# Optimization experiments

Hardware: AMD Instinct MI355X
Metric: run time of the kernel (lower is better)

Reference implementation:

```python
import jax, jax.numpy as jnp
import numpy as np

BLOCK = 128          # per-block quantization group size (BLOCK_SIZE in source)
FP8_MAX = 448.0      # max representable magnitude of float8_e4m3fn


def _quantize(x2d):
    # Per-128-element block quantization along the last (contiguous) dim,
    # matching quantize_fp8_triton applied to the row-major flattened tensor.
    R, K = x2d.shape
    xb = x2d.reshape(R, K // BLOCK, BLOCK)
    s = jnp.max(jnp.abs(xb), axis=-1) / FP8_MAX            # [R, K//BLOCK] fp32 scales
    y = (xb / s[..., None]).astype(jnp.float8_e4m3fn)      # fp8 payload
    return y, s


def _dequantize(y, s):
    # Inline dequant: fp8 -> fp32 times per-block scale (fused into GEMM accum in the kernel).
    return (y.astype(jnp.float32) * s[..., None]).reshape(y.shape[0], -1)


def setup_inputs() -> dict:
    key = jax.random.key(0)
    kx, kw = jax.random.split(key)
    B, T, D, O = 4, 2048, 4096, 4096
    x = jax.random.normal(kx, (B, T, D), dtype=jnp.float32)
    limit = float(np.sqrt(6.0 / (D + O)))  # xavier_uniform_
    weight = jax.random.uniform(kw, (O, D), minval=-limit, maxval=limit, dtype=jnp.float32)
    return {"x": x, "weight": weight}


def reference(x, weight):
    B, T, D = x.shape
    xf = x.reshape(-1, D)                  # [M, K]
    xq, xs = _quantize(xf)                 # fp8 activations + per-(row,kblock) scales
    wq, ws = _quantize(weight)             # fp8 weights + per-(row,kblock) scales
    # Block-scaled GEMM: sum_i (A_i @ B_i^T) * a_s[:, i] * b_s[:, i]
    # expressed equivalently as dequant-then-matmul (identical math, fp32 accumulate).
    out = _dequantize(xq, xs) @ _dequantize(wq, ws).T      # [M, N]
    return out.reshape(B, T, -1)
```

## Files before the change

kernel.cpp:

```cpp
#include <hip/hip_runtime.h>

using u16 = unsigned short;
typedef int i32x4 __attribute__((ext_vector_type(4)));
typedef int i32x8 __attribute__((ext_vector_type(8)));
typedef float f32x4 __attribute__((ext_vector_type(4)));
typedef float f32x2 __attribute__((ext_vector_type(2)));
typedef float f32x16 __attribute__((ext_vector_type(16)));

#define SC1 0x7F7F7F7F

__device__ inline void async16(const void* g, void* l) {
    __builtin_amdgcn_global_load_lds(
        (__attribute__((address_space(1))) void*)(g),
        (__attribute__((address_space(3))) void*)(l),
        16, 0, 0);
}

__device__ inline i32x8 mk8(i32x4 lo, i32x4 hi) {
    return __builtin_shufflevector(lo, hi, 0, 1, 2, 3, 4, 5, 6, 7);
}

__global__ void quant_kernel(const float* __restrict__ in,
                             u16* __restrict__ outq,
                             float* __restrict__ outs,
                             long R) {
    long wid = (long)blockIdx.x * 4 + (threadIdx.x >> 6);
    int lane = threadIdx.x & 63;
    if (wid >= R * 32) return;

    float2 v = reinterpret_cast<const float2*>(in + wid * 128)[lane];
    float a = fmaxf(fabsf(v.x), fabsf(v.y));
#pragma unroll
    for (int off = 32; off; off >>= 1) a = fmaxf(a, __shfl_xor(a, off));

    float s = a / 448.0f;
    float qx = v.x / s;
    float qy = v.y / s;
    qx = fminf(fmaxf(qx, -448.0f), 448.0f);
    qy = fminf(fmaxf(qy, -448.0f), 448.0f);

    int pk = __builtin_amdgcn_cvt_pk_fp8_f32(qx, qy, 0, false);
    outq[wid * 64 + lane] = (u16)(pk & 0xFFFF);

    if (lane == 0) {
        long row = wid >> 5, kb = wid & 31;
        outs[kb * R + row] = s;
    }
}


#define SWZ(x) ((x) ^ ((((x) >> 7) & 7) << 4))

#define FENCE asm volatile("" ::: "memory");
#define BARRIER { __builtin_amdgcn_s_barrier(); FENCE }
#define VMC0 { asm volatile("s_waitcnt vmcnt(0)" ::: "memory"); }

__global__ __launch_bounds__(256, 2) void gemm_fp8(
    const char* __restrict__ Aq, const char* __restrict__ Bq,
    const float* __restrict__ AscaleG, const float* __restrict__ BscaleG,
    float* __restrict__ C, int M, int N) {
    extern __shared__ __align__(16) char smem[];
    const int KBYTES = 4096;

    const int tid = threadIdx.x;
    const int wid = tid >> 6;
    const int lane = tid & 63;
    const int l31 = lane & 31;
    const int lh = lane >> 5;
    const int wr2 = wid >> 1;
    const int wc2 = wid & 1;

    int nwg = gridDim.x, bid = blockIdx.x, swz = bid;
    if ((nwg & 7) == 0) swz = (bid & 7) * (nwg >> 3) + (bid >> 3);
    const int nbn = N >> 7;
    const long brow = (long)(swz / nbn) << 7;
    const long bcol = (long)(swz % nbn) << 7;

    const char* Abase = Aq + brow * KBYTES;
    const char* Bbase = Bq + bcol * KBYTES;

    int aofs[4];
#pragma unroll
    for (int c = 0; c < 4; ++c) {
        int dloc = c * 4096 + tid * 16;
        int l = SWZ(dloc);
        aofs[c] = (l >> 7) * KBYTES + (l & 127);
    }

    int cox[4];
#pragma unroll
    for (int kh = 0; kh < 2; ++kh)
#pragma unroll
        for (int hh = 0; hh < 2; ++hh)
            cox[kh * 2 + hh] =
                (((kh << 6) | (lh << 5) | (hh << 4)) ^ ((lane & 7) << 4));

    int arowb[2], brownn[2];
#pragma unroll
    for (int rb = 0; rb < 2; ++rb) arowb[rb] = (wr2 * 64 + rb * 32 + l31) << 7;
#pragma unroll
    for (int n = 0; n < 2; ++n) brownn[n] = (wc2 * 64 + n * 32 + l31) << 7;

#define STAGE(kb1) { int bufb_ = (kb1) & 1; \
    _Pragma("unroll") for (int c_ = 0; c_ < 4; ++c_) { \
        char* dA_ = smem + bufb_ * 16384 + c_ * 4096 + wid * 1024; \
        async16(Abase + aofs[c_] + (long)(kb1) * 128, dA_); \
        async16(Bbase + aofs[c_] + (long)(kb1) * 128, dA_ + 32768); } \
    if (wid == 0 && lane < 32) \
        async16((const char*)AscaleG + ((long)(kb1) * M + brow) * 4 + lane * 16, \
                smem + 65536 + bufb_ * 512); \
    if (wid == 1 && lane < 32) \
        async16((const char*)BscaleG + ((long)(kb1) * N + bcol) * 4 + lane * 16, \
                smem + 66560 + bufb_ * 512); }

    f32x16 acc[2][2];
#pragma unroll
    for (int rb = 0; rb < 2; ++rb)
#pragma unroll
        for (int n = 0; n < 2; ++n)
#pragma unroll
            for (int e = 0; e < 16; ++e) acc[rb][n][e] = 0.f;

    STAGE(0);
    VMC0; BARRIER;

    for (int kb = 0; kb < 32; ++kb) {
        const int buf = kb & 1;
        if (kb < 31) STAGE(kb + 1);

        const char* Ab = smem + buf * 16384;
        const char* Bb = smem + 32768 + buf * 16384;
        const float* Sa = (const float*)(smem + 65536 + buf * 512);
        const float* Sb = (const float*)(smem + 66560 + buf * 512);

        i32x8 bfr[2][2];
#pragma unroll
        for (int n = 0; n < 2; ++n)
#pragma unroll
            for (int kh = 0; kh < 2; ++kh)
                bfr[n][kh] = mk8(*(const i32x4*)(Bb + brownn[n] + cox[kh * 2]),
                                 *(const i32x4*)(Bb + brownn[n] + cox[kh * 2 + 1]));
        float sbv[2];
#pragma unroll
        for (int n = 0; n < 2; ++n) sbv[n] = Sb[wc2 * 64 + n * 32 + l31];

#pragma unroll
        for (int rb = 0; rb < 2; ++rb) {
            i32x8 a0 = mk8(*(const i32x4*)(Ab + arowb[rb] + cox[0]),
                           *(const i32x4*)(Ab + arowb[rb] + cox[1]));
            i32x8 a1 = mk8(*(const i32x4*)(Ab + arowb[rb] + cox[2]),
                           *(const i32x4*)(Ab + arowb[rb] + cox[3]));
            f32x4 sa4[4];
#pragma unroll
            for (int i = 0; i < 4; ++i)
                sa4[i] = *(const f32x4*)(Sa + wr2 * 64 + rb * 32 + 4 * lh + 8 * i);
            __builtin_amdgcn_s_setprio(1);
            f32x16 t0 = __builtin_amdgcn_mfma_scale_f32_32x32x64_f8f6f4(
                a0, bfr[0][0], (f32x16)(0.f), 0, 0, 0, SC1, 0, SC1);
            t0 = __builtin_amdgcn_mfma_scale_f32_32x32x64_f8f6f4(
                a1, bfr[0][1], t0, 0, 0, 0, SC1, 0, SC1);
            f32x16 t1 = __builtin_amdgcn_mfma_scale_f32_32x32x64_f8f6f4(
                a0, bfr[1][0], (f32x16)(0.f), 0, 0, 0, SC1, 0, SC1);
            t1 = __builtin_amdgcn_mfma_scale_f32_32x32x64_f8f6f4(
                a1, bfr[1][1], t1, 0, 0, 0, SC1, 0, SC1);
            __builtin_amdgcn_s_setprio(0);
#pragma unroll
            for (int i = 0; i < 4; ++i)
#pragma unroll
                for (int j = 0; j < 4; ++j) {
                    acc[rb][0][i * 4 + j] = fmaf(t0[i * 4 + j],
                        sa4[i][j] * sbv[0], acc[rb][0][i * 4 + j]);
                    acc[rb][1][i * 4 + j] = fmaf(t1[i * 4 + j],
                        sa4[i][j] * sbv[1], acc[rb][1][i * 4 + j]);
                }
        }

        VMC0; BARRIER;
    }

#pragma unroll
    for (int rb = 0; rb < 2; ++rb)
#pragma unroll
        for (int n = 0; n < 2; ++n)
#pragma unroll
            for (int e = 0; e < 16; ++e) {
                long r = brow + wr2 * 64 + rb * 32 + (e & 3) + 8 * (e >> 2) + 4 * lh;
                long cc = bcol + wc2 * 64 + n * 32 + l31;
                C[r * (long)N + cc] = acc[rb][n][e];
            }
#undef STAGE
}

extern "C" void kernel_launch(void* const* d_in, const int* in_sizes, int n_in,
                              void* d_out, int out_size, void* d_ws, size_t ws_size,
                              hipStream_t stream) {
    const float* x = (const float*)d_in[0];
    const float* w = (const float*)d_in[1];
    float* out = (float*)d_out;

    const int K = 4096;
    const long M = (long)in_sizes[0] / K;
    const long N = (long)in_sizes[1] / K;

    u16* Aq = (u16*)d_ws;
    u16* Bq = Aq + (size_t)M * K / 2;
    float* Asc = (float*)(Bq + (size_t)N * K / 2);
    float* Bsc = Asc + 32 * (size_t)M;

    const long nblkA = M * 32, nblkB = N * 32;
    quant_kernel<<<dim3((unsigned)((nblkA + 3) / 4)), dim3(256), 0, stream>>>(
        x, Aq, Asc, M);
    quant_kernel<<<dim3((unsigned)((nblkB + 3) / 4)), dim3(256), 0, stream>>>(
        w, Bq, Bsc, N);

    static int smem_set = 0;
    if (!smem_set) {
        hipFuncSetAttribute((const void*)gemm_fp8,
                            hipFuncAttributeMaxDynamicSharedMemorySize, 67584);
        smem_set = 1;
    }
    dim3 grid((unsigned)((M / 128) * (N / 128)));
    gemm_fp8<<<grid, dim3(256), 67584, stream>>>(
        (const char*)Aq, (const char*)Bq, Asc, Bsc, out, (int)M, (int)N);
}
```

Before: 275.0 us.

## Shrink GEMM tile to 128x64, fuse quant launches, raise occupancy

After: 300.8 us. +9.4%, slower.

```diff
diff --git a/kernel.cpp b/kernel.cpp
--- a/kernel.cpp
+++ b/kernel.cpp
@@ -20,15 +20,20 @@
     return __builtin_shufflevector(lo, hi, 0, 1, 2, 3, 4, 5, 6, 7);
 }
 
-__global__ void quant_kernel(const float* __restrict__ in,
-                             u16* __restrict__ outq,
-                             float* __restrict__ outs,
-                             long R) {
+__global__ void quant_kernel(const float* __restrict__ x,
+                             const float* __restrict__ w,
+                             u16* __restrict__ Aq, u16* __restrict__ Bq,
+                             float* __restrict__ Asc, float* __restrict__ Bsc,
+                             long nA, long nTot, long MM, long NN) {
     long wid = (long)blockIdx.x * 4 + (threadIdx.x >> 6);
     int lane = threadIdx.x & 63;
-    if (wid >= R * 32) return;
-
-    float2 v = reinterpret_cast<const float2*>(in + wid * 128)[lane];
+    if (wid >= nTot) return;
+
+    const float* in; u16* outq; float* outs; long R, id;
+    if (wid < nA) { in = x; outq = Aq; outs = Asc; R = MM; id = wid; }
+    else          { in = w; outq = Bq; outs = Bsc; R = NN; id = wid - nA; }
+
+    float2 v = reinterpret_cast<const float2*>(in + id * 128)[lane];
     float a = fmaxf(fabsf(v.x), fabsf(v.y));
 #pragma unroll
     for (int off = 32; off; off >>= 1) a = fmaxf(a, __shfl_xor(a, off));
@@ -40,10 +45,10 @@
     qy = fminf(fmaxf(qy, -448.0f), 448.0f);
 
     int pk = __builtin_amdgcn_cvt_pk_fp8_f32(qx, qy, 0, false);
-    outq[wid * 64 + lane] = (u16)(pk & 0xFFFF);
+    outq[id * 64 + lane] = (u16)(pk & 0xFFFF);
 
     if (lane == 0) {
-        long row = wid >> 5, kb = wid & 31;
+        long row = id >> 5, kb = id & 31;
         outs[kb * R + row] = s;
     }
 }
@@ -55,7 +60,7 @@
 #define BARRIER { __builtin_amdgcn_s_barrier(); FENCE }
 #define VMC0 { asm volatile("s_waitcnt vmcnt(0)" ::: "memory"); }
 
-__global__ __launch_bounds__(256, 2) void gemm_fp8(
+__global__ __launch_bounds__(256, 3) void gemm_fp8(
     const char* __restrict__ Aq, const char* __restrict__ Bq,
     const float* __restrict__ AscaleG, const float* __restrict__ BscaleG,
     float* __restrict__ C, int M, int N) {
@@ -72,9 +77,9 @@
 
     int nwg = gridDim.x, bid = blockIdx.x, swz = bid;
     if ((nwg & 7) == 0) swz = (bid & 7) * (nwg >> 3) + (bid >> 3);
-    const int nbn = N >> 7;
+    const int nbn = N >> 6;
     const long brow = (long)(swz / nbn) << 7;
-    const long bcol = (long)(swz % nbn) << 7;
+    const long bcol = (long)(swz % nbn) << 6;
 
     const char* Abase = Aq + brow * KBYTES;
     const char* Bbase = Bq + bcol * KBYTES;
@@ -95,31 +100,30 @@
             cox[kh * 2 + hh] =
                 (((kh << 6) | (lh << 5) | (hh << 4)) ^ ((lane & 7) << 4));
 
-    int arowb[2], brownn[2];
+    int arowb[2];
 #pragma unroll
     for (int rb = 0; rb < 2; ++rb) arowb[rb] = (wr2 * 64 + rb * 32 + l31) << 7;
-#pragma unroll
-    for (int n = 0; n < 2; ++n) brownn[n] = (wc2 * 64 + n * 32 + l31) << 7;
+    const int brown = (wc2 * 32 + l31) << 7;
 
 #define STAGE(kb1) { int bufb_ = (kb1) & 1; \
     _Pragma("unroll") for (int c_ = 0; c_ < 4; ++c_) { \
         char* dA_ = smem + bufb_ * 16384 + c_ * 4096 + wid * 1024; \
-        async16(Abase + aofs[c_] + (long)(kb1) * 128, dA_); \
-        async16(Bbase + aofs[c_] + (long)(kb1) * 128, dA_ + 32768); } \
+        async16(Abase + aofs[c_] + (long)(kb1) * 128, dA_); } \
+    _Pragma("unroll") for (int c_ = 0; c_ < 2; ++c_) { \
+        char* dB_ = smem + 32768 + bufb_ * 8192 + c_ * 4096 + wid * 1024; \
+        async16(Bbase + aofs[c_] + (long)(kb1) * 128, dB_); } \
     if (wid == 0 && lane < 32) \
         async16((const char*)AscaleG + ((long)(kb1) * M + brow) * 4 + lane * 16, \
-                smem + 65536 + bufb_ * 512); \
-    if (wid == 1 && lane < 32) \
+                smem + 49152 + bufb_ * 512); \
+    if (wid == 3 && lane < 16) \
         async16((const char*)BscaleG + ((long)(kb1) * N + bcol) * 4 + lane * 16, \
-                smem + 66560 + bufb_ * 512); }
-
-    f32x16 acc[2][2];
+                smem + 50176 + bufb_ * 256); }
+
+    f32x2 acc2[2][8];
 #pragma unroll
     for (int rb = 0; rb < 2; ++rb)
 #pragma unroll
-        for (int n = 0; n < 2; ++n)
-#pragma unroll
-            for (int e = 0; e < 16; ++e) acc[rb][n][e] = 0.f;
+        for (int p = 0; p < 8; ++p) acc2[rb][p] = (f32x2){0.f, 0.f};
 
     STAGE(0);
     VMC0; BARRIER;
@@ -129,20 +133,16 @@
         if (kb < 31) STAGE(kb + 1);
 
         const char* Ab = smem + buf * 16384;
-        const char* Bb = smem + 32768 + buf * 16384;
-        const float* Sa = (const float*)(smem + 65536 + buf * 512);
-        const float* Sb = (const float*)(smem + 66560 + buf * 512);
-
-        i32x8 bfr[2][2];
-#pragma unroll
-        for (int n = 0; n < 2; ++n)
-#pragma unroll
-            for (int kh = 0; kh < 2; ++kh)
-                bfr[n][kh] = mk8(*(const i32x4*)(Bb + brownn[n] + cox[kh * 2]),
-                                 *(const i32x4*)(Bb + brownn[n] + cox[kh * 2 + 1]));
-        float sbv[2];
-#pragma unroll
-        for (int n = 0; n < 2; ++n) sbv[n] = Sb[wc2 * 64 + n * 32 + l31];
+        const char* Bb = smem + 32768 + buf * 8192;
+        const float* Sa = (const float*)(smem + 49152 + buf * 512);
+        const float* Sb = (const float*)(smem + 50176 + buf * 256);
+
+        i32x8 bfr[2];
+#pragma unroll
+        for (int kh = 0; kh < 2; ++kh)
+            bfr[kh] = mk8(*(const i32x4*)(Bb + brown + cox[kh * 2]),
+                          *(const i32x4*)(Bb + brown + cox[kh * 2 + 1]));
+        const float sbv = Sb[wc2 * 32 + l31];
 
 #pragma unroll
         for (int rb = 0; rb < 2; ++rb) {
@@ -155,23 +155,18 @@
             for (int i = 0; i < 4; ++i)
                 sa4[i] = *(const f32x4*)(Sa + wr2 * 64 + rb * 32 + 4 * lh + 8 * i);
             __builtin_amdgcn_s_setprio(1);
-            f32x16 t0 = __builtin_amdgcn_mfma_scale_f32_32x32x64_f8f6f4(
-                a0, bfr[0][0], (f32x16)(0.f), 0, 0, 0, SC1, 0, SC1);
-            t0 = __builtin_amdgcn_mfma_scale_f32_32x32x64_f8f6f4(
-                a1, bfr[0][1], t0, 0, 0, 0, SC1, 0, SC1);
-            f32x16 t1 = __builtin_amdgcn_mfma_scale_f32_32x32x64_f8f6f4(
-                a0, bfr[1][0], (f32x16)(0.f), 0, 0, 0, SC1, 0, SC1);
-            t1 = __builtin_amdgcn_mfma_scale_f32_32x32x64_f8f6f4(
-                a1, bfr[1][1], t1, 0, 0, 0, SC1, 0, SC1);
+            f32x16 t = __builtin_amdgcn_mfma_scale_f32_32x32x64_f8f6f4(
+                a0, bfr[0], (f32x16)(0.f), 0, 0, 0, SC1, 0, SC1);
+            t = __builtin_amdgcn_mfma_scale_f32_32x32x64_f8f6f4(
+                a1, bfr[1], t, 0, 0, 0, SC1, 0, SC1);
             __builtin_amdgcn_s_setprio(0);
 #pragma unroll
             for (int i = 0; i < 4; ++i)
 #pragma unroll
-                for (int j = 0; j < 4; ++j) {
-                    acc[rb][0][i * 4 + j] = fmaf(t0[i * 4 + j],
-                        sa4[i][j] * sbv[0], acc[rb][0][i * 4 + j]);
-                    acc[rb][1][i * 4 + j] = fmaf(t1[i * 4 + j],
-                        sa4[i][j] * sbv[1], acc[rb][1][i * 4 + j]);
+                for (int jh = 0; jh < 2; ++jh) {
+                    f32x2 sp = (f32x2){sa4[i][2 * jh], sa4[i][2 * jh + 1]} * sbv;
+                    f32x2 tv = (f32x2){t[i * 4 + 2 * jh], t[i * 4 + 2 * jh + 1]};
+                    acc2[rb][i * 2 + jh] = tv * sp + acc2[rb][i * 2 + jh];
                 }
         }
 
@@ -181,13 +176,16 @@
 #pragma unroll
     for (int rb = 0; rb < 2; ++rb)
 #pragma unroll
-        for (int n = 0; n < 2; ++n)
-#pragma unroll
-            for (int e = 0; e < 16; ++e) {
-                long r = brow + wr2 * 64 + rb * 32 + (e & 3) + 8 * (e >> 2) + 4 * lh;
-                long cc = bcol + wc2 * 64 + n * 32 + l31;
-                C[r * (long)N + cc] = acc[rb][n][e];
-            }
+        for (int i = 0; i < 4; ++i)
+#pragma unroll
+            for (int jh = 0; jh < 2; ++jh)
+#pragma unroll
+                for (int w = 0; w < 2; ++w) {
+                    int j = 2 * jh + w;
+                    long r = brow + wr2 * 64 + rb * 32 + j + 8 * i + 4 * lh;
+                    long cc = bcol + wc2 * 32 + l31;
+                    C[r * (long)N + cc] = acc2[rb][i * 2 + jh][w];
+                }
 #undef STAGE
 }
 
@@ -207,19 +205,17 @@
     float* Asc = (float*)(Bq + (size_t)N * K / 2);
     float* Bsc = Asc + 32 * (size_t)M;
 
-    const long nblkA = M * 32, nblkB = N * 32;
-    quant_kernel<<<dim3((unsigned)((nblkA + 3) / 4)), dim3(256), 0, stream>>>(
-        x, Aq, Asc, M);
-    quant_kernel<<<dim3((unsigned)((nblkB + 3) / 4)), dim3(256), 0, stream>>>(
-        w, Bq, Bsc, N);
+    const long nA = M * 32, nB = N * 32;
+    quant_kernel<<<dim3((unsigned)((nA + nB + 3) / 4)), dim3(256), 0, stream>>>(
+        x, w, Aq, Bq, Asc, Bsc, nA, nA + nB, M, N);
 
     static int smem_set = 0;
     if (!smem_set) {
         hipFuncSetAttribute((const void*)gemm_fp8,
-                            hipFuncAttributeMaxDynamicSharedMemorySize, 67584);
+                            hipFuncAttributeMaxDynamicSharedMemorySize, 50688);
         smem_set = 1;
     }
-    dim3 grid((unsigned)((M / 128) * (N / 128)));
-    gemm_fp8<<<grid, dim3(256), 67584, stream>>>(
+    dim3 grid((unsigned)((M / 128) * (N / 64)));
+    gemm_fp8<<<grid, dim3(256), 50688, stream>>>(
         (const char*)Aq, (const char*)Bq, Asc, Bsc, out, (int)M, (int)N);
 }
```
